# Kernel optimization log

Hardware: AMD Instinct MI355X
Metric: run time of the kernel (lower is better)

Reference implementation:

```python
import jax, jax.numpy as jnp
import numpy as np

DIM = 256
HEADS = 8
HEAD_DIM = DIM // HEADS  # 32
LN_EPS = 1e-5


def setup_inputs() -> dict:
    key = jax.random.key(0)
    ks = jax.random.split(key, 11)
    B, N = 8, 4096
    s = 1.0 / np.sqrt(DIM)
    return {
        "q": jax.random.normal(ks[0], (B, N, DIM), dtype=jnp.float32),
        "k": jax.random.normal(ks[1], (B, N, DIM), dtype=jnp.float32),
        "v": jax.random.normal(ks[2], (B, N, DIM), dtype=jnp.float32),
        "Wq": jax.random.normal(ks[3], (DIM, DIM), dtype=jnp.float32) * s,
        "bq": jax.random.normal(ks[4], (DIM,), dtype=jnp.float32) * 0.01,
        "Wk": jax.random.normal(ks[5], (DIM, DIM), dtype=jnp.float32) * s,
        "bk": jax.random.normal(ks[6], (DIM,), dtype=jnp.float32) * 0.01,
        "Wv": jax.random.normal(ks[7], (DIM, DIM), dtype=jnp.float32) * s,
        "bv": jax.random.normal(ks[8], (DIM,), dtype=jnp.float32) * 0.01,
        "ln_gamma": jnp.ones((DIM,), dtype=jnp.float32),
        "ln_beta": jnp.zeros((DIM,), dtype=jnp.float32),
    }


def _heads(x, B, N):
    # [B, N, DIM] -> [B, HEADS, N, HEAD_DIM]
    return x.reshape(B, N, HEADS, HEAD_DIM).transpose(0, 2, 1, 3)


def reference(q, k, v, Wq, bq, Wk, bk, Wv, bv, ln_gamma, ln_beta):
    B, N, _ = q.shape
    ql = _heads(q @ Wq.T + bq, B, N)
    kl = _heads(k @ Wk.T + bk, B, N)
    vl = _heads(v @ Wv.T + bv, B, N)

    # FFT-domain "attention": rfft2 over (seq, head_dim), complex multiply, irfft2
    q_fft = jnp.fft.rfft2(ql.astype(jnp.float32))   # [B, H, N, HEAD_DIM//2+1] complex
    k_fft = jnp.fft.rfft2(kl.astype(jnp.float32))
    attention = jnp.fft.irfft2(q_fft * k_fft)        # [B, H, N, HEAD_DIM]
    attention = jax.nn.softmax(attention, axis=-1)

    out = vl * attention                             # elementwise value gate
    out = out.transpose(0, 2, 1, 3).reshape(B, N, HEADS * HEAD_DIM)

    # dropout is identity at eval; residual + LayerNorm(256)
    out = out + v
    mu = jnp.mean(out, axis=-1, keepdims=True)
    var = jnp.var(out, axis=-1, keepdims=True)
    out = (out - mu) * jax.lax.rsqrt(var + LN_EPS) * ln_gamma + ln_beta
    return out
```

## Files before the change

kernel.cpp:

```cpp
#include <hip/hip_runtime.h>

#define NFREQ 2049

using cf = float2;
typedef __attribute__((ext_vector_type(8))) short short8;
typedef __attribute__((ext_vector_type(4))) float floatx4;

__device__ inline unsigned short bf16_rne(float x) {
  unsigned u = __float_as_uint(x);
  unsigned r = u + 0x7FFFu + ((u >> 16) & 1u);
  return (unsigned short)(r >> 16);
}
__device__ inline float bf16_to_f(unsigned short h) {
  return __uint_as_float(((unsigned)h) << 16);
}
__device__ inline cf cmul(cf a, cf b) {
  return make_float2(a.x * b.x - a.y * b.y, a.x * b.y + a.y * b.x);
}
__device__ inline cf cadd(cf a, cf b) { return make_float2(a.x + b.x, a.y + b.y); }
__device__ inline cf csub(cf a, cf b) { return make_float2(a.x - b.x, a.y - b.y); }

__global__ __launch_bounds__(256, 4) void gemm_proj(
    const float* __restrict__ Xq, const float* __restrict__ Wq, const float* __restrict__ bq,
    const float* __restrict__ Xk, const float* __restrict__ Wk, const float* __restrict__ bk,
    const float* __restrict__ Xv, const float* __restrict__ Wv, const float* __restrict__ bv,
    float* __restrict__ dq, float* __restrict__ dk, float* __restrict__ dv)
{
  const int z = blockIdx.z;
  const float* X = (z == 0) ? Xq : (z == 1) ? Xk : Xv;
  const float* W = (z == 0) ? Wq : (z == 1) ? Wk : Wv;
  const float* bias = (z == 0) ? bq : (z == 1) ? bk : bv;
  float* dst = (z == 0) ? dq : (z == 1) ? dk : dv;

  __shared__ __align__(16) unsigned short sm[12416];
  unsigned short* sAhi = sm;
  unsigned short* sAlo = sm + 4128;
  unsigned short* sBhi = sm + 8256;
  unsigned short* sBlo = sm + 10336;

  const int tid = threadIdx.x;
  const int m0 = blockIdx.x * 128;
  const int j0 = blockIdx.y * 64;
  const int wave = tid >> 6, lane = tid & 63;
  const int wm = wave & 1, wj = wave >> 1;
  const int lm = lane & 15, quad = lane >> 4;

  floatx4 acc[4][2] = {};

  for (int k0 = 0; k0 < 256; k0 += 32) {
    float4 xa[4], wb[2];
    #pragma unroll
    for (int r = 0; r < 4; r++) {
      int v = tid + r * 256;
      int row = v >> 3, c4 = (v & 7) * 4;
      xa[r] = *(const float4*)(X + (size_t)(m0 + row) * 256 + k0 + c4);
    }
    #pragma unroll
    for (int r = 0; r < 2; r++) {
      int v = tid + r * 256;
      int row = v >> 3, c4 = (v & 7) * 4;
      wb[r] = *(const float4*)(W + (size_t)(j0 + row) * 256 + k0 + c4);
    }
    __syncthreads();
    #pragma unroll
    for (int r = 0; r < 4; r++) {
      int v = tid + r * 256;
      int row = v >> 3, c4 = (v & 7) * 4;
      int q = c4 >> 3, off = c4 & 7;
      float f[4] = {xa[r].x, xa[r].y, xa[r].z, xa[r].w};
      unsigned short h[4], l[4];
      #pragma unroll
      for (int i = 0; i < 4; i++) {
        h[i] = bf16_rne(f[i]);
        l[i] = bf16_rne(f[i] - bf16_to_f(h[i]));
      }
      int idx = ((q * 129 + row) << 3) + off;
      *(uint2*)&sAhi[idx] = make_uint2((unsigned)h[0] | ((unsigned)h[1] << 16),
                                       (unsigned)h[2] | ((unsigned)h[3] << 16));
      *(uint2*)&sAlo[idx] = make_uint2((unsigned)l[0] | ((unsigned)l[1] << 16),
                                       (unsigned)l[2] | ((unsigned)l[3] << 16));
    }
    #pragma unroll
    for (int r = 0; r < 2; r++) {
      int v = tid + r * 256;
      int row = v >> 3, c4 = (v & 7) * 4;
      int q = c4 >> 3, off = c4 & 7;
      float f[4] = {wb[r].x, wb[r].y, wb[r].z, wb[r].w};
      unsigned short h[4], l[4];
      #pragma unroll
      for (int i = 0; i < 4; i++) {
        h[i] = bf16_rne(f[i]);
        l[i] = bf16_rne(f[i] - bf16_to_f(h[i]));
      }
      int idx = ((q * 65 + row) << 3) + off;
      *(uint2*)&sBhi[idx] = make_uint2((unsigned)h[0] | ((unsigned)h[1] << 16),
                                       (unsigned)h[2] | ((unsigned)h[3] << 16));
      *(uint2*)&sBlo[idx] = make_uint2((unsigned)l[0] | ((unsigned)l[1] << 16),
                                       (unsigned)l[2] | ((unsigned)l[3] << 16));
    }
    __syncthreads();

    short8 ahi[4], alo[4], bhi[2], blo[2];
    #pragma unroll
    for (int mf = 0; mf < 4; mf++) {
      int row = wm * 64 + mf * 16 + lm;
      int idx = ((quad * 129 + row) << 3);
      ahi[mf] = *(const short8*)&sAhi[idx];
      alo[mf] = *(const short8*)&sAlo[idx];
    }
    #pragma unroll
    for (int jf = 0; jf < 2; jf++) {
      int row = wj * 32 + jf * 16 + lm;
      int idx = ((quad * 65 + row) << 3);
      bhi[jf] = *(const short8*)&sBhi[idx];
      blo[jf] = *(const short8*)&sBlo[idx];
    }
    #pragma unroll
    for (int mf = 0; mf < 4; mf++)
      #pragma unroll
      for (int jf = 0; jf < 2; jf++) {
        acc[mf][jf] = __builtin_amdgcn_mfma_f32_16x16x32_bf16(
            ahi[mf], bhi[jf], acc[mf][jf], 0, 0, 0);
        acc[mf][jf] = __builtin_amdgcn_mfma_f32_16x16x32_bf16(
            ahi[mf], blo[jf], acc[mf][jf], 0, 0, 0);
        acc[mf][jf] = __builtin_amdgcn_mfma_f32_16x16x32_bf16(
            alo[mf], bhi[jf], acc[mf][jf], 0, 0, 0);
      }
  }

  #pragma unroll
  for (int jf = 0; jf < 2; jf++) {
    float bj = bias[j0 + wj * 32 + jf * 16 + lm];
    #pragma unroll
    for (int mf = 0; mf < 4; mf++)
      #pragma unroll
      for (int r = 0; r < 4; r++)
        acc[mf][jf][r] += bj;
  }

  if (z == 2) {
    #pragma unroll
    for (int mf = 0; mf < 4; mf++)
      #pragma unroll
      for (int jf = 0; jf < 2; jf++) {
        int j = j0 + wj * 32 + jf * 16 + lm;
        int mb = m0 + wm * 64 + mf * 16 + quad * 4;
        #pragma unroll
        for (int r = 0; r < 4; r++)
          dst[(size_t)(mb + r) * 256 + j] = acc[mf][jf][r];
      }
  } else {
    const int b = m0 >> 12;
    const int n0 = m0 & 4095;
    #pragma unroll
    for (int mf = 0; mf < 4; mf++)
      #pragma unroll
      for (int jf = 0; jf < 2; jf++) {
        int j = j0 + wj * 32 + jf * 16 + lm;
        int nb = n0 + wm * 64 + mf * 16 + quad * 4;
        float4 o = make_float4(acc[mf][jf][0], acc[mf][jf][1],
                               acc[mf][jf][2], acc[mf][jf][3]);
        *(float4*)(dst + (size_t)(b * 256 + j) * 4096 + nb) = o;
      }
  }
}

#define FFT_LDS 4376

__device__ inline int swz(int i) { return i + (i >> 4) + (i >> 8) + (i >> 9); }
__device__ inline int digrev8(int n) {
  return ((n & 7) << 9) | (((n >> 3) & 7) << 6) | (((n >> 6) & 7) << 3) | ((n >> 9) & 7);
}

template<int SIGN>
__device__ inline void fft8_stages(cf* X, int tid)
{
  const float C = 0.70710678118654752f;
  const float sg = (float)SIGN;
  #pragma unroll
  for (int s = 0; s < 4; s++) {
    const int q = 1 << (3 * s);
    __syncthreads();
    #pragma unroll
    for (int r = 0; r < 2; r++) {
      int t = tid + r * 256;
      int j = t & (q - 1);
      int base = ((t >> (3 * s)) << (3 * s + 3)) + j;
      cf x[8];
      #pragma unroll
      for (int l = 0; l < 8; l++) x[l] = X[swz(base + l * q)];
      if (s > 0) {
        float a = sg * 6.283185307179586f * (float)j / (float)(8 * q);
        float sn, cs;
        __sincosf(a, &sn, &cs);
        cf w1 = make_float2(cs, sn);
        cf w = w1;
        #pragma unroll
        for (int l = 1; l < 8; l++) {
          x[l] = cmul(x[l], w);
          if (l < 7) w = cmul(w, w1);
        }
      }
      cf u0 = cadd(x[0], x[4]), v0 = csub(x[0], x[4]);
      cf u1 = cadd(x[1], x[5]), v1 = csub(x[1], x[5]);
      cf u2 = cadd(x[2], x[6]), v2 = csub(x[2], x[6]);
      cf u3 = cadd(x[3], x[7]), v3 = csub(x[3], x[7]);
      cf w1v = make_float2(C * (v1.x - sg * v1.y), C * (v1.y + sg * v1.x));
      cf w2v = make_float2(-sg * v2.y, sg * v2.x);
      cf w3v = make_float2(C * (-v3.x - sg * v3.y), C * (sg * v3.x - v3.y));
      cf e0 = cadd(u0, u2), e1 = csub(u0, u2);
      cf o0 = cadd(u1, u3), o1 = csub(u1, u3);
      cf F0 = cadd(e0, o0), F4 = csub(e0, o0);
      cf F2 = make_float2(e1.x - sg * o1.y, e1.y + sg * o1.x);
      cf F6 = make_float2(e1.x + sg * o1.y, e1.y - sg * o1.x);
      cf e0b = cadd(v0, w2v), e1b = csub(v0, w2v);
      cf o0b = cadd(w1v, w3v), o1b = csub(w1v, w3v);
      cf F1 = cadd(e0b, o0b), F5 = csub(e0b, o0b);
      cf F3 = make_float2(e1b.x - sg * o1b.y, e1b.y + sg * o1b.x);
      cf F7 = make_float2(e1b.x + sg * o1b.y, e1b.y - sg * o1b.x);
      X[swz(base + 0 * q)] = F0;
      X[swz(base + 1 * q)] = F1;
      X[swz(base + 2 * q)] = F2;
      X[swz(base + 3 * q)] = F3;
      X[swz(base + 4 * q)] = F4;
      X[swz(base + 5 * q)] = F5;
      X[swz(base + 6 * q)] = F6;
      X[swz(base + 7 * q)] = F7;
    }
  }
  __syncthreads();
}

__global__ __launch_bounds__(256) void fft_fwd(
    const float* __restrict__ srcQ, cf* __restrict__ dstQ,
    const float* __restrict__ srcK, cf* __restrict__ dstK)
{
  __shared__ cf X[FFT_LDS];
  const float* src_base = blockIdx.y ? srcK : srcQ;
  cf* dst_base = blockIdx.y ? dstK : dstQ;
  const int c0 = blockIdx.x * 2;
  const float* s0 = src_base + (size_t)c0 * 4096;
  const float* s1 = s0 + 4096;
  const int tid = threadIdx.x;
  #pragma unroll
  for (int i = 0; i < 16; i++) {
    int n = tid + i * 256;
    X[swz(digrev8(n))] = make_float2(s0[n], s1[n]);
  }
  fft8_stages<-1>(X, tid);
  cf* d0 = dst_base + (size_t)c0 * NFREQ;
  cf* d1 = d0 + NFREQ;
  for (int f = tid; f <= 2048; f += 256) {
    cf Zf = X[swz(f)];
    cf Zm = X[swz((4096 - f) & 4095)];
    d0[f] = make_float2(0.5f * (Zf.x + Zm.x), 0.5f * (Zf.y - Zm.y));
    d1[f] = make_float2(0.5f * (Zf.y + Zm.y), 0.5f * (Zm.x - Zf.x));
  }
}

__device__ inline cf tw_f(int l, int h) {
  int j = l & (h - 1);
  if (l & h) {
    float sn, cs;
    __sincosf(-3.14159265358979f * (float)j / (float)h, &sn, &cs);
    return make_float2(cs, sn);
  }
  return make_float2(1.0f, 0.0f);
}

template<int H>
__device__ inline cf fwd_stage(cf x, cf w, float sg) {
  float px = __shfl_xor(x.x, H);
  float py = __shfl_xor(x.y, H);
  return cmul(make_float2(px + sg * x.x, py + sg * x.y), w);
}
template<int H>
__device__ inline cf inv_stage(cf x, cf w, float sg) {
  cf t = cmul(x, w);
  float px = __shfl_xor(t.x, H);
  float py = __shfl_xor(t.y, H);
  return make_float2(px + sg * t.x, py + sg * t.y);
}
template<int H>
__device__ inline cf nt_stage(cf x, float sg) {
  float px = __shfl_xor(x.x, H);
  float py = __shfl_xor(x.y, H);
  return make_float2(px + sg * x.x, py + sg * x.y);
}

__global__ __launch_bounds__(256) void freq_conv(
    cf* __restrict__ Qf, const cf* __restrict__ Kf)
{
  __shared__ cf Qs[32][65];
  __shared__ cf Ks[32][65];
  const int f0 = blockIdx.x * 64;
  const int bh = blockIdx.y;
  const int tid = threadIdx.x;
  const int wave = tid >> 6, lane = tid & 63;
  const int d = lane & 31, hl = lane >> 5;

  #pragma unroll
  for (int i = 0; i < 8; i++) {
    int v = tid + i * 256;
    int e = v >> 6, fl = v & 63;
    int f = f0 + fl;
    if (f < NFREQ) {
      Qs[e][fl] = Qf[(size_t)(bh * 32 + e) * NFREQ + f];
      Ks[e][fl] = Kf[(size_t)(bh * 32 + e) * NFREQ + f];
    } else {
      Qs[e][fl] = make_float2(0.0f, 0.0f);
      Ks[e][fl] = make_float2(0.0f, 0.0f);
    }
  }
  __syncthreads();

  const cf w16 = tw_f(d, 16), w8 = tw_f(d, 8), w4 = tw_f(d, 4), w2 = tw_f(d, 2);
  const float s16 = (d & 16) ? -1.0f : 1.0f;
  const float s8  = (d & 8)  ? -1.0f : 1.0f;
  const float s4  = (d & 4)  ? -1.0f : 1.0f;
  const float s2  = (d & 2)  ? -1.0f : 1.0f;
  const float s1  = (d & 1)  ? -1.0f : 1.0f;

  #pragma unroll
  for (int it = 0; it < 8; it++) {
    const int fl = it * 8 + wave * 2 + hl;
    cf q = Qs[d][fl];
    cf k = Ks[d][fl];
    q = fwd_stage<16>(q, w16, s16);  k = fwd_stage<16>(k, w16, s16);
    q = fwd_stage<8>(q, w8, s8);     k = fwd_stage<8>(k, w8, s8);
    q = fwd_stage<4>(q, w4, s4);     k = fwd_stage<4>(k, w4, s4);
    q = fwd_stage<2>(q, w2, s2);     k = fwd_stage<2>(k, w2, s2);
    q = nt_stage<1>(q, s1);          k = nt_stage<1>(k, s1);
    cf c = cmul(q, k);
    c = nt_stage<1>(c, s1);
    c = inv_stage<2>(c, make_float2(w2.x, -w2.y), s2);
    c = inv_stage<4>(c, make_float2(w4.x, -w4.y), s4);
    c = inv_stage<8>(c, make_float2(w8.x, -w8.y), s8);
    c = inv_stage<16>(c, make_float2(w16.x, -w16.y), s16);
    Qs[d][fl] = make_float2(c.x * (1.0f / 32.0f), c.y * (1.0f / 32.0f));
  }
  __syncthreads();

  #pragma unroll
  for (int i = 0; i < 8; i++) {
    int v = tid + i * 256;
    int e = v >> 6, fl = v & 63;
    int f = f0 + fl;
    if (f < NFREQ)
      Qf[(size_t)(bh * 32 + e) * NFREQ + f] = Qs[e][fl];
  }
}

__global__ __launch_bounds__(256) void fft_inv(
    const cf* __restrict__ Cf, float* __restrict__ attn)
{
  __shared__ cf X[FFT_LDS];
  const int c0 = blockIdx.x * 2;
  const cf* s0 = Cf + (size_t)c0 * NFREQ;
  const cf* s1 = s0 + NFREQ;
  const int tid = threadIdx.x;
  for (int f = tid; f <= 2048; f += 256) {
    cf c1 = s0[f];
    cf c2 = s1[f];
    X[swz(digrev8(f))] = make_float2(c1.x - c2.y, c1.y + c2.x);
    if (f != 0 && f != 2048)
      X[swz(digrev8(4096 - f))] = make_float2(c1.x + c2.y, c2.x - c1.y);
  }
  fft8_stages<+1>(X, tid);
  float* d0 = attn + (size_t)c0 * 4096;
  float* d1 = d0 + 4096;
  const float inv = 1.0f / 4096.0f;
  #pragma unroll
  for (int i = 0; i < 16; i++) {
    int n = tid + i * 256;
    cf z = X[swz(n)];
    d0[n] = z.x * inv;
    d1[n] = z.y * inv;
  }
}

__global__ __launch_bounds__(256) void finalize_kernel(
    const float* __restrict__ attn, const float* __restrict__ VL,
    const float* __restrict__ vin, const float* __restrict__ gamma,
    const float* __restrict__ beta, float* __restrict__ out)
{
  __shared__ float At[256][33];
  const int n0 = blockIdx.x * 32;
  const int b = blockIdx.y;
  const int tid = threadIdx.x;
  #pragma unroll
  for (int i = 0; i < 32; i++) {
    int v = tid + i * 256;
    int hd = v >> 5, nn = v & 31;
    At[hd][nn] = attn[(size_t)(b * 256 + hd) * 4096 + n0 + nn];
  }
  __syncthreads();
  const int wave = tid >> 6, lane = tid & 63;
  float g[4], bt[4];
  #pragma unroll
  for (int r = 0; r < 4; r++) { g[r] = gamma[64 * r + lane]; bt[r] = beta[64 * r + lane]; }

  for (int t = 0; t < 8; t++) {
    const int nn = wave * 8 + t;
    const int n = n0 + nn;
    float p[4];
    #pragma unroll
    for (int r = 0; r < 4; r++) {
      float a = At[64 * r + lane][nn];
      float mx = a;
      #pragma unroll
      for (int off = 16; off >= 1; off >>= 1) mx = fmaxf(mx, __shfl_xor(mx, off, 32));
      float e = __expf(a - mx);
      float s = e;
      #pragma unroll
      for (int off = 16; off >= 1; off >>= 1) s += __shfl_xor(s, off, 32);
      p[r] = e / s;
    }
    const size_t base = ((size_t)b * 4096 + n) * 256 + lane;
    float o[4];
    float s1 = 0.0f, s2 = 0.0f;
    #pragma unroll
    for (int r = 0; r < 4; r++) {
      o[r] = VL[base + 64 * r] * p[r] + vin[base + 64 * r];
      s1 += o[r];
      s2 += o[r] * o[r];
    }
    #pragma unroll
    for (int off = 32; off >= 1; off >>= 1) {
      s1 += __shfl_xor(s1, off, 64);
      s2 += __shfl_xor(s2, off, 64);
    }
    float mu = s1 * (1.0f / 256.0f);
    float var = s2 * (1.0f / 256.0f) - mu * mu;
    float rs = rsqrtf(var + 1e-5f);
    #pragma unroll
    for (int r = 0; r < 4; r++)
      out[base + 64 * r] = (o[r] - mu) * rs * g[r] + bt[r];
  }
}

extern "C" void kernel_launch(void* const* d_in, const int* in_sizes, int n_in,
                              void* d_out, int out_size, void* d_ws, size_t ws_size,
                              hipStream_t stream)
{
  const float* q  = (const float*)d_in[0];
  const float* k  = (const float*)d_in[1];
  const float* v  = (const float*)d_in[2];
  const float* Wq = (const float*)d_in[3];
  const float* bq = (const float*)d_in[4];
  const float* Wk = (const float*)d_in[5];
  const float* bk = (const float*)d_in[6];
  const float* Wv = (const float*)d_in[7];
  const float* bv = (const float*)d_in[8];
  const float* ln_gamma = (const float*)d_in[9];
  const float* ln_beta  = (const float*)d_in[10];
  float* out = (float*)d_out;

  float* ws = (float*)d_ws;
  float* QL = ws;
  float* KL = QL + (size_t)8388608;
  float* VL = KL + (size_t)8388608;
  cf* Qf = (cf*)(VL + (size_t)8388608);
  cf* Kf = Qf + (size_t)2048 * NFREQ;
  float* attn = QL;

  gemm_proj<<<dim3(256, 4, 3), 256, 0, stream>>>(q, Wq, bq, k, Wk, bk, v, Wv, bv,
                                                 QL, KL, VL);

  fft_fwd<<<dim3(1024, 2), 256, 0, stream>>>(QL, Qf, KL, Kf);

  freq_conv<<<dim3(33, 64), 256, 0, stream>>>(Qf, Kf);

  fft_inv<<<1024, 256, 0, stream>>>(Qf, attn);

  finalize_kernel<<<dim3(128, 8), 256, 0, stream>>>(attn, VL, v, ln_gamma,
                                                    ln_beta, out);
}
```

Baseline: 289.1 us.

## Prefetch next GEMM K-tile into registers and use packed bf16 conversion

```diff
diff --git a/kernel.cpp b/kernel.cpp
--- a/kernel.cpp
+++ b/kernel.cpp
@@ -13,6 +13,11 @@
 }
 __device__ inline float bf16_to_f(unsigned short h) {
   return __uint_as_float(((unsigned)h) << 16);
+}
+__device__ inline unsigned pk_bf16(float a, float b) {
+  unsigned r;
+  asm("v_cvt_pk_bf16_f32 %0, %1, %2" : "=v"(r) : "v"(a), "v"(b));
+  return r;
 }
 __device__ inline cf cmul(cf a, cf b) {
   return make_float2(a.x * b.x - a.y * b.y, a.x * b.y + a.y * b.x);
@@ -47,57 +52,77 @@
 
   floatx4 acc[4][2] = {};
 
+  int aIdx[4], bIdx[2];
+  const float* aSrc[4];
+  const float* bSrc[2];
+  #pragma unroll
+  for (int r = 0; r < 4; r++) {
+    int v = tid + r * 256;
+    int row = v >> 3, c4 = (v & 7) * 4;
+    int q = c4 >> 3, off = c4 & 7;
+    aIdx[r] = ((q * 129 + row) << 3) + off;
+    aSrc[r] = X + (size_t)(m0 + row) * 256 + c4;
+  }
+  #pragma unroll
+  for (int r = 0; r < 2; r++) {
+    int v = tid + r * 256;
+    int row = v >> 3, c4 = (v & 7) * 4;
+    int q = c4 >> 3, off = c4 & 7;
+    bIdx[r] = ((q * 65 + row) << 3) + off;
+    bSrc[r] = W + (size_t)(j0 + row) * 256 + c4;
+  }
+
+  float4 xa[4], wb[2];
+  #pragma unroll
+  for (int r = 0; r < 4; r++) xa[r] = *(const float4*)(aSrc[r]);
+  #pragma unroll
+  for (int r = 0; r < 2; r++) wb[r] = *(const float4*)(bSrc[r]);
+
   for (int k0 = 0; k0 < 256; k0 += 32) {
-    float4 xa[4], wb[2];
+    uint2 ahv[4], alv[4], bhv[2], blv[2];
     #pragma unroll
     for (int r = 0; r < 4; r++) {
-      int v = tid + r * 256;
-      int row = v >> 3, c4 = (v & 7) * 4;
-      xa[r] = *(const float4*)(X + (size_t)(m0 + row) * 256 + k0 + c4);
+      unsigned h01 = pk_bf16(xa[r].x, xa[r].y);
+      unsigned h23 = pk_bf16(xa[r].z, xa[r].w);
+      float l0 = xa[r].x - __uint_as_float(h01 << 16);
+      float l1 = xa[r].y - __uint_as_float(h01 & 0xFFFF0000u);
+      float l2 = xa[r].z - __uint_as_float(h23 << 16);
+      float l3 = xa[r].w - __uint_as_float(h23 & 0xFFFF0000u);
+      ahv[r] = make_uint2(h01, h23);
+      alv[r] = make_uint2(pk_bf16(l0, l1), pk_bf16(l2, l3));
     }
     #pragma unroll
     for (int r = 0; r < 2; r++) {
-      int v = tid + r * 256;
-      int row = v >> 3, c4 = (v & 7) * 4;
-      wb[r] = *(const float4*)(W + (size_t)(j0 + row) * 256 + k0 + c4);
-    }
+      unsigned h01 = pk_bf16(wb[r].x, wb[r].y);
+      unsigned h23 = pk_bf16(wb[r].z, wb[r].w);
+      float l0 = wb[r].x - __uint_as_float(h01 << 16);
+      float l1 = wb[r].y - __uint_as_float(h01 & 0xFFFF0000u);
+      float l2 = wb[r].z - __uint_as_float(h23 << 16);
+      float l3 = wb[r].w - __uint_as_float(h23 & 0xFFFF0000u);
+      bhv[r] = make_uint2(h01, h23);
+      blv[r] = make_uint2(pk_bf16(l0, l1), pk_bf16(l2, l3));
+    }
+
     __syncthreads();
+
     #pragma unroll
     for (int r = 0; r < 4; r++) {
-      int v = tid + r * 256;
-      int row = v >> 3, c4 = (v & 7) * 4;
-      int q = c4 >> 3, off = c4 & 7;
-      float f[4] = {xa[r].x, xa[r].y, xa[r].z, xa[r].w};
-      unsigned short h[4], l[4];
-      #pragma unroll
-      for (int i = 0; i < 4; i++) {
-        h[i] = bf16_rne(f[i]);
-        l[i] = bf16_rne(f[i] - bf16_to_f(h[i]));
-      }
-      int idx = ((q * 129 + row) << 3) + off;
-      *(uint2*)&sAhi[idx] = make_uint2((unsigned)h[0] | ((unsigned)h[1] << 16),
-                                       (unsigned)h[2] | ((unsigned)h[3] << 16));
-      *(uint2*)&sAlo[idx] = make_uint2((unsigned)l[0] | ((unsigned)l[1] << 16),
-                                       (unsigned)l[2] | ((unsigned)l[3] << 16));
+      *(uint2*)&sAhi[aIdx[r]] = ahv[r];
+      *(uint2*)&sAlo[aIdx[r]] = alv[r];
     }
     #pragma unroll
     for (int r = 0; r < 2; r++) {
-      int v = tid + r * 256;
-      int row = v >> 3, c4 = (v & 7) * 4;
-      int q = c4 >> 3, off = c4 & 7;
-      float f[4] = {wb[r].x, wb[r].y, wb[r].z, wb[r].w};
-      unsigned short h[4], l[4];
-      #pragma unroll
-      for (int i = 0; i < 4; i++) {
-        h[i] = bf16_rne(f[i]);
-        l[i] = bf16_rne(f[i] - bf16_to_f(h[i]));
-      }
-      int idx = ((q * 65 + row) << 3) + off;
-      *(uint2*)&sBhi[idx] = make_uint2((unsigned)h[0] | ((unsigned)h[1] << 16),
-                                       (unsigned)h[2] | ((unsigned)h[3] << 16));
-      *(uint2*)&sBlo[idx] = make_uint2((unsigned)l[0] | ((unsigned)l[1] << 16),
-                                       (unsigned)l[2] | ((unsigned)l[3] << 16));
-    }
+      *(uint2*)&sBhi[bIdx[r]] = bhv[r];
+      *(uint2*)&sBlo[bIdx[r]] = blv[r];
+    }
+
+    if (k0 < 224) {
+      #pragma unroll
+      for (int r = 0; r < 4; r++) xa[r] = *(const float4*)(aSrc[r] + k0 + 32);
+      #pragma unroll
+      for (int r = 0; r < 2; r++) wb[r] = *(const float4*)(bSrc[r] + k0 + 32);
+    }
+
     __syncthreads();
 
     short8 ahi[4], alo[4], bhi[2], blo[2];
```

Measured after the change: 282.6 us. -2.3%, faster.

## Pre-split weights to bf16 hi/lo once and double-buffer activation tiles

Applied to the files above, without the earlier changes.

```diff
diff --git a/kernel.cpp b/kernel.cpp
--- a/kernel.cpp
+++ b/kernel.cpp
@@ -14,29 +14,59 @@
 __device__ inline float bf16_to_f(unsigned short h) {
   return __uint_as_float(((unsigned)h) << 16);
 }
+__device__ inline unsigned pk_bf16(float a, float b) {
+  unsigned r;
+  asm("v_cvt_pk_bf16_f32 %0, %1, %2" : "=v"(r) : "v"(a), "v"(b));
+  return r;
+}
 __device__ inline cf cmul(cf a, cf b) {
   return make_float2(a.x * b.x - a.y * b.y, a.x * b.y + a.y * b.x);
 }
 __device__ inline cf cadd(cf a, cf b) { return make_float2(a.x + b.x, a.y + b.y); }
 __device__ inline cf csub(cf a, cf b) { return make_float2(a.x - b.x, a.y - b.y); }
 
+__global__ __launch_bounds__(256) void wconv(
+    const float* __restrict__ Wq, const float* __restrict__ Wk,
+    const float* __restrict__ Wv,
+    unsigned short* __restrict__ Whi, unsigned short* __restrict__ Wlo)
+{
+  int g = blockIdx.x * 256 + threadIdx.x;
+  int c = g & 31, j = (g >> 5) & 255, z = g >> 13;
+  const float* W = (z == 0) ? Wq : (z == 1) ? Wk : Wv;
+  const float* s = W + (size_t)j * 256 + c * 8;
+  float4 f0 = *(const float4*)s;
+  float4 f1 = *(const float4*)(s + 4);
+  unsigned h01 = pk_bf16(f0.x, f0.y), h23 = pk_bf16(f0.z, f0.w);
+  unsigned h45 = pk_bf16(f1.x, f1.y), h67 = pk_bf16(f1.z, f1.w);
+  float l0 = f0.x - __uint_as_float(h01 << 16);
+  float l1 = f0.y - __uint_as_float(h01 & 0xFFFF0000u);
+  float l2 = f0.z - __uint_as_float(h23 << 16);
+  float l3 = f0.w - __uint_as_float(h23 & 0xFFFF0000u);
+  float l4 = f1.x - __uint_as_float(h45 << 16);
+  float l5 = f1.y - __uint_as_float(h45 & 0xFFFF0000u);
+  float l6 = f1.z - __uint_as_float(h67 << 16);
+  float l7 = f1.w - __uint_as_float(h67 & 0xFFFF0000u);
+  size_t base = ((size_t)z * 8192 + c * 256 + j) * 8;
+  *(uint4*)&Whi[base] = make_uint4(h01, h23, h45, h67);
+  *(uint4*)&Wlo[base] = make_uint4(pk_bf16(l0, l1), pk_bf16(l2, l3),
+                                   pk_bf16(l4, l5), pk_bf16(l6, l7));
+}
+
 __global__ __launch_bounds__(256, 4) void gemm_proj(
-    const float* __restrict__ Xq, const float* __restrict__ Wq, const float* __restrict__ bq,
-    const float* __restrict__ Xk, const float* __restrict__ Wk, const float* __restrict__ bk,
-    const float* __restrict__ Xv, const float* __restrict__ Wv, const float* __restrict__ bv,
+    const float* __restrict__ Xq, const float* __restrict__ bq,
+    const float* __restrict__ Xk, const float* __restrict__ bk,
+    const float* __restrict__ Xv, const float* __restrict__ bv,
+    const unsigned short* __restrict__ Whi, const unsigned short* __restrict__ Wlo,
     float* __restrict__ dq, float* __restrict__ dk, float* __restrict__ dv)
 {
   const int z = blockIdx.z;
   const float* X = (z == 0) ? Xq : (z == 1) ? Xk : Xv;
-  const float* W = (z == 0) ? Wq : (z == 1) ? Wk : Wv;
   const float* bias = (z == 0) ? bq : (z == 1) ? bk : bv;
   float* dst = (z == 0) ? dq : (z == 1) ? dk : dv;
-
-  __shared__ __align__(16) unsigned short sm[12416];
-  unsigned short* sAhi = sm;
-  unsigned short* sAlo = sm + 4128;
-  unsigned short* sBhi = sm + 8256;
-  unsigned short* sBlo = sm + 10336;
+  const unsigned short* WhiZ = Whi + (size_t)z * 65536;
+  const unsigned short* WloZ = Wlo + (size_t)z * 65536;
+
+  __shared__ __align__(16) unsigned short sm[2][8256];
 
   const int tid = threadIdx.x;
   const int m0 = blockIdx.x * 128;
@@ -47,74 +77,97 @@
 
   floatx4 acc[4][2] = {};
 
-  for (int k0 = 0; k0 < 256; k0 += 32) {
-    float4 xa[4], wb[2];
-    #pragma unroll
-    for (int r = 0; r < 4; r++) {
-      int v = tid + r * 256;
-      int row = v >> 3, c4 = (v & 7) * 4;
-      xa[r] = *(const float4*)(X + (size_t)(m0 + row) * 256 + k0 + c4);
-    }
-    #pragma unroll
-    for (int r = 0; r < 2; r++) {
-      int v = tid + r * 256;
-      int row = v >> 3, c4 = (v & 7) * 4;
-      wb[r] = *(const float4*)(W + (size_t)(j0 + row) * 256 + k0 + c4);
-    }
-    __syncthreads();
-    #pragma unroll
-    for (int r = 0; r < 4; r++) {
-      int v = tid + r * 256;
-      int row = v >> 3, c4 = (v & 7) * 4;
-      int q = c4 >> 3, off = c4 & 7;
-      float f[4] = {xa[r].x, xa[r].y, xa[r].z, xa[r].w};
-      unsigned short h[4], l[4];
-      #pragma unroll
-      for (int i = 0; i < 4; i++) {
-        h[i] = bf16_rne(f[i]);
-        l[i] = bf16_rne(f[i] - bf16_to_f(h[i]));
-      }
-      int idx = ((q * 129 + row) << 3) + off;
-      *(uint2*)&sAhi[idx] = make_uint2((unsigned)h[0] | ((unsigned)h[1] << 16),
-                                       (unsigned)h[2] | ((unsigned)h[3] << 16));
-      *(uint2*)&sAlo[idx] = make_uint2((unsigned)l[0] | ((unsigned)l[1] << 16),
-                                       (unsigned)l[2] | ((unsigned)l[3] << 16));
-    }
-    #pragma unroll
-    for (int r = 0; r < 2; r++) {
-      int v = tid + r * 256;
-      int row = v >> 3, c4 = (v & 7) * 4;
-      int q = c4 >> 3, off = c4 & 7;
-      float f[4] = {wb[r].x, wb[r].y, wb[r].z, wb[r].w};
-      unsigned short h[4], l[4];
-      #pragma unroll
-      for (int i = 0; i < 4; i++) {
-        h[i] = bf16_rne(f[i]);
-        l[i] = bf16_rne(f[i] - bf16_to_f(h[i]));
-      }
-      int idx = ((q * 65 + row) << 3) + off;
-      *(uint2*)&sBhi[idx] = make_uint2((unsigned)h[0] | ((unsigned)h[1] << 16),
-                                       (unsigned)h[2] | ((unsigned)h[3] << 16));
-      *(uint2*)&sBlo[idx] = make_uint2((unsigned)l[0] | ((unsigned)l[1] << 16),
-                                       (unsigned)l[2] | ((unsigned)l[3] << 16));
-    }
-    __syncthreads();
-
-    short8 ahi[4], alo[4], bhi[2], blo[2];
+  int sIdx[2];
+  const float* aSrc[2];
+  #pragma unroll
+  for (int r = 0; r < 2; r++) {
+    int v = tid + r * 256;
+    int row = v >> 2, q = v & 3;
+    sIdx[r] = (q * 129 + row) << 3;
+    aSrc[r] = X + (size_t)(m0 + row) * 256 + q * 8;
+  }
+
+  float4 xa[2][2];
+  #pragma unroll
+  for (int r = 0; r < 2; r++) {
+    xa[r][0] = *(const float4*)(aSrc[r]);
+    xa[r][1] = *(const float4*)(aSrc[r] + 4);
+  }
+  #pragma unroll
+  for (int r = 0; r < 2; r++) {
+    float4 f0 = xa[r][0], f1 = xa[r][1];
+    unsigned h01 = pk_bf16(f0.x, f0.y), h23 = pk_bf16(f0.z, f0.w);
+    unsigned h45 = pk_bf16(f1.x, f1.y), h67 = pk_bf16(f1.z, f1.w);
+    float l0 = f0.x - __uint_as_float(h01 << 16);
+    float l1 = f0.y - __uint_as_float(h01 & 0xFFFF0000u);
+    float l2 = f0.z - __uint_as_float(h23 << 16);
+    float l3 = f0.w - __uint_as_float(h23 & 0xFFFF0000u);
+    float l4 = f1.x - __uint_as_float(h45 << 16);
+    float l5 = f1.y - __uint_as_float(h45 & 0xFFFF0000u);
+    float l6 = f1.z - __uint_as_float(h67 << 16);
+    float l7 = f1.w - __uint_as_float(h67 & 0xFFFF0000u);
+    *(uint4*)&sm[0][sIdx[r]] = make_uint4(h01, h23, h45, h67);
+    *(uint4*)&sm[0][4128 + sIdx[r]] = make_uint4(pk_bf16(l0, l1), pk_bf16(l2, l3),
+                                                 pk_bf16(l4, l5), pk_bf16(l6, l7));
+  }
+  #pragma unroll
+  for (int r = 0; r < 2; r++) {
+    xa[r][0] = *(const float4*)(aSrc[r] + 32);
+    xa[r][1] = *(const float4*)(aSrc[r] + 36);
+  }
+  __syncthreads();
+
+  for (int ks = 0; ks < 8; ks++) {
+    const int p = ks & 1;
+
+    short8 bhi[2], blo[2];
+    #pragma unroll
+    for (int jf = 0; jf < 2; jf++) {
+      int c = ks * 4 + quad;
+      int j = j0 + wj * 32 + jf * 16 + lm;
+      size_t off = ((size_t)c * 256 + j) * 8;
+      bhi[jf] = *(const short8*)&WhiZ[off];
+      blo[jf] = *(const short8*)&WloZ[off];
+    }
+
+    short8 ahi[4], alo[4];
     #pragma unroll
     for (int mf = 0; mf < 4; mf++) {
       int row = wm * 64 + mf * 16 + lm;
-      int idx = ((quad * 129 + row) << 3);
-      ahi[mf] = *(const short8*)&sAhi[idx];
-      alo[mf] = *(const short8*)&sAlo[idx];
-    }
-    #pragma unroll
-    for (int jf = 0; jf < 2; jf++) {
-      int row = wj * 32 + jf * 16 + lm;
-      int idx = ((quad * 65 + row) << 3);
-      bhi[jf] = *(const short8*)&sBhi[idx];
-      blo[jf] = *(const short8*)&sBlo[idx];
-    }
+      int idx = (quad * 129 + row) << 3;
+      ahi[mf] = *(const short8*)&sm[p][idx];
+      alo[mf] = *(const short8*)&sm[p][4128 + idx];
+    }
+
+    if (ks < 7) {
+      #pragma unroll
+      for (int r = 0; r < 2; r++) {
+        float4 f0 = xa[r][0], f1 = xa[r][1];
+        unsigned h01 = pk_bf16(f0.x, f0.y), h23 = pk_bf16(f0.z, f0.w);
+        unsigned h45 = pk_bf16(f1.x, f1.y), h67 = pk_bf16(f1.z, f1.w);
+        float l0 = f0.x - __uint_as_float(h01 << 16);
+        float l1 = f0.y - __uint_as_float(h01 & 0xFFFF0000u);
+        float l2 = f0.z - __uint_as_float(h23 << 16);
+        float l3 = f0.w - __uint_as_float(h23 & 0xFFFF0000u);
+        float l4 = f1.x - __uint_as_float(h45 << 16);
+        float l5 = f1.y - __uint_as_float(h45 & 0xFFFF0000u);
+        float l6 = f1.z - __uint_as_float(h67 << 16);
+        float l7 = f1.w - __uint_as_float(h67 & 0xFFFF0000u);
+        *(uint4*)&sm[p ^ 1][sIdx[r]] = make_uint4(h01, h23, h45, h67);
+        *(uint4*)&sm[p ^ 1][4128 + sIdx[r]] =
+            make_uint4(pk_bf16(l0, l1), pk_bf16(l2, l3),
+                       pk_bf16(l4, l5), pk_bf16(l6, l7));
+      }
+      if (ks < 6) {
+        #pragma unroll
+        for (int r = 0; r < 2; r++) {
+          const float* s = aSrc[r] + (ks + 2) * 32;
+          xa[r][0] = *(const float4*)s;
+          xa[r][1] = *(const float4*)(s + 4);
+        }
+      }
+    }
+
     #pragma unroll
     for (int mf = 0; mf < 4; mf++)
       #pragma unroll
@@ -126,6 +179,8 @@
         acc[mf][jf] = __builtin_amdgcn_mfma_f32_16x16x32_bf16(
             alo[mf], bhi[jf], acc[mf][jf], 0, 0, 0);
       }
+
+    __syncthreads();
   }
 
   #pragma unroll
@@ -464,8 +519,13 @@
   cf* Kf = Qf + (size_t)2048 * NFREQ;
   float* attn = QL;
 
-  gemm_proj<<<dim3(256, 4, 3), 256, 0, stream>>>(q, Wq, bq, k, Wk, bk, v, Wv, bv,
-                                                 QL, KL, VL);
+  unsigned short* Whi = (unsigned short*)Kf;
+  unsigned short* Wlo = Whi + (size_t)3 * 65536;
+
+  wconv<<<96, 256, 0, stream>>>(Wq, Wk, Wv, Whi, Wlo);
+
+  gemm_proj<<<dim3(256, 4, 3), 256, 0, stream>>>(q, bq, k, bk, v, bv,
+                                                 Whi, Wlo, QL, KL, VL);
 
   fft_fwd<<<dim3(1024, 2), 256, 0, stream>>>(QL, Qf, KL, Kf);
 
```

Measured after the change: 289.6 us. Within noise of the previous version (+0.2%).
